# Optimization experiments

Hardware: AMD Instinct MI355X
Metric: run time of the kernel (lower is better)

Reference implementation:

```python
import jax, jax.numpy as jnp
import numpy as np

N = 50000      # nodes
E = 800000     # edges (avg degree 16)
G = 1024       # graphs in batch
C = 128        # hidden / interaction channels
FIN = 16       # num_node_features
FE = 3         # num_edge_features
L = 3          # num_interactions
CUTOFF = 10.0
LOG2 = float(np.log(2.0))
BN_EPS = 1e-5

def ssp(v):
    # ShiftedSoftplus: softplus(x) - log(2)
    return jax.nn.softplus(v) - LOG2

def setup_inputs() -> dict:
    key = jax.random.key(0)
    ks = jax.random.split(key, 24)
    s = 0.05
    inp = {}
    inp["x"] = jax.random.normal(ks[0], (N, FIN), jnp.float32)
    inp["edge_index"] = jax.random.randint(ks[1], (2, E), 0, N, dtype=jnp.int32)
    inp["edge_weight"] = jax.random.uniform(ks[2], (E,), jnp.float32) * CUTOFF
    inp["edge_attr"] = jax.random.normal(ks[3], (E, FE), jnp.float32)
    inp["batch"] = jnp.sort(jax.random.randint(ks[4], (N,), 0, G, dtype=jnp.int32))
    # node embedding (node_data='x'): Linear(FIN,C) -> Linear(C,C)
    inp["W_l1"] = jax.random.normal(ks[5], (FIN, C), jnp.float32) * s
    inp["b_l1"] = jnp.zeros((C,), jnp.float32)
    inp["W_l2"] = jax.random.normal(ks[6], (C, C), jnp.float32) * s
    inp["b_l2"] = jnp.zeros((C,), jnp.float32)
    # BatchNorm1d affine params
    inp["bn_g"] = jnp.ones((C,), jnp.float32)
    inp["bn_b"] = jnp.zeros((C,), jnp.float32)
    # L stacked interaction layers (SchNet-style CFConv)
    inp["Wi_in"] = jax.random.normal(ks[7], (L, C, C), jnp.float32) * s
    inp["bi_in"] = jnp.zeros((L, C), jnp.float32)
    inp["We1"] = jax.random.normal(ks[8], (L, FE, C), jnp.float32) * s
    inp["be1"] = jnp.zeros((L, C), jnp.float32)
    inp["We2"] = jax.random.normal(ks[9], (L, C, C), jnp.float32) * s
    inp["be2"] = jnp.zeros((L, C), jnp.float32)
    inp["Wi_out"] = jax.random.normal(ks[10], (L, C, C), jnp.float32) * s
    inp["bi_out"] = jnp.zeros((L, C), jnp.float32)
    # GeneralReadOutLayer (128,'sum',32,1): pool -> Linear(128,32)+SSP -> Linear(32,1)+SSP
    inp["W_r1"] = jax.random.normal(ks[11], (C, 32), jnp.float32) * s
    inp["b_r1"] = jnp.zeros((32,), jnp.float32)
    inp["W_r2"] = jax.random.normal(ks[12], (32, 1), jnp.float32) * s
    inp["b_r2"] = jnp.zeros((1,), jnp.float32)
    return inp

def _forward(x, edge_weight, edge_attr,
             W_l1, b_l1, W_l2, b_l2, bn_g, bn_b,
             Wi_in, bi_in, We1, be1, We2, be2, Wi_out, bi_out,
             W_r1, b_r1, W_r2, b_r2, edge_index, batch):
    src, dst = edge_index[0], edge_index[1]
    # node embedding: Linear -> Linear
    h = (x @ W_l1 + b_l1) @ W_l2 + b_l2                   # [N, C]
    # BatchNorm1d (training-mode batch stats over nodes)
    mu = jnp.mean(h, axis=0)
    var = jnp.var(h, axis=0)
    h = (h - mu) * jax.lax.rsqrt(var + BN_EPS) * bn_g + bn_b
    # cosine cutoff envelope on edge distances
    env = 0.5 * (jnp.cos(edge_weight * (jnp.pi / CUTOFF)) + 1.0)  # [E]
    # GeoResNet: residual stack of interactions
    for i in range(L):
        filt = ssp(edge_attr @ We1[i] + be1[i]) @ We2[i] + be2[i]   # [E, C]
        hin = h @ Wi_in[i] + bi_in[i]                               # [N, C]
        msg = hin[src] * filt * env[:, None]                        # [E, C] gather
        agg = jax.ops.segment_sum(msg, dst, num_segments=N)         # [N, C] scatter
        h = h + ssp(agg @ Wi_out[i] + bi_out[i])
    # GeneralReadOutLayer: segment 'sum' pool then MLP with SSP
    hg = jax.ops.segment_sum(h, batch, num_segments=G)              # [G, C]
    out = ssp(hg @ W_r1 + b_r1)
    out = ssp(out @ W_r2 + b_r2)                                    # [G, 1]
    return out.reshape(-1)                                          # [G]

def reference(x, edge_index, edge_weight, edge_attr, batch,
              W_l1, b_l1, W_l2, b_l2, bn_g, bn_b,
              Wi_in, bi_in, We1, be1, We2, be2, Wi_out, bi_out,
              W_r1, b_r1, W_r2, b_r2):
    return _forward(x, edge_weight, edge_attr,
                    W_l1, b_l1, W_l2, b_l2, bn_g, bn_b,
                    Wi_in, bi_in, We1, be1, We2, be2, Wi_out, bi_out,
                    W_r1, b_r1, W_r2, b_r2, edge_index, batch)
```

## Files before the change

kernel.cpp:

```cpp
#include <hip/hip_runtime.h>
#include <hip/hip_bf16.h>
#include <math.h>

#define N_NODES 50000
#define N_EDGES 800000
#define N_GRAPH 1024
#define CDIM 128
#define FINDIM 16
#define NL 3
#define WTP 132

using short8  = __attribute__((ext_vector_type(8))) short;
using floatx4 = __attribute__((ext_vector_type(4))) float;

__device__ __forceinline__ float sspf(float x) {
    return __logf(1.0f + __expf(x)) - 0.6931471805599453f;
}

__device__ __forceinline__ unsigned short f2bf(float f) {
    unsigned int u = __float_as_uint(f);
    u = u + 0x7FFFu + ((u >> 16) & 1u);
    return (unsigned short)(u >> 16);
}

__device__ __forceinline__ float bf2f(unsigned short h) {
    return __uint_as_float((unsigned int)h << 16);
}

__device__ __forceinline__ unsigned int packbf(float a, float b) {
    __hip_bfloat162 h = __float22bfloat162_rn(make_float2(a, b));
    return *(unsigned int*)&h;
}

__device__ __forceinline__ short8 ldfrag(const unsigned short* WT, int c, int k0) {
    const uint2* p = (const uint2*)(WT + c * WTP + k0);
    short8 r;
    *(uint2*)&r       = p[0];
    *((uint2*)&r + 1) = p[1];
    return r;
}

__global__ void k_fuse(const float* __restrict__ Wl1, const float* __restrict__ bl1,
                       const float* __restrict__ Wl2, const float* __restrict__ bl2,
                       float* __restrict__ Wf, float* __restrict__ bfv) {
    for (int o = threadIdx.x; o < FINDIM * CDIM + CDIM; o += 256) {
        if (o < FINDIM * CDIM) {
            int f = o >> 7, c = o & 127;
            float s = 0.f;
            for (int k = 0; k < CDIM; ++k) s += Wl1[f * CDIM + k] * Wl2[k * CDIM + c];
            Wf[o] = s;
        } else {
            int c = o - FINDIM * CDIM;
            float s = bl2[c];
            for (int k = 0; k < CDIM; ++k) s += bl1[k] * Wl2[k * CDIM + c];
            bfv[c] = s;
        }
    }
}

__global__ void k_embed_bn(const float* __restrict__ x, const float* __restrict__ Wf,
                           const float* __restrict__ bfv, float* __restrict__ h,
                           float* __restrict__ bnsum) {
    __shared__ float wfs[FINDIM * CDIM];
    __shared__ float bfs[CDIM];
    __shared__ float sd[512];
    for (int o = threadIdx.x; o < FINDIM * CDIM; o += 256) wfs[o] = Wf[o];
    if (threadIdx.x < CDIM) bfs[threadIdx.x] = bfv[threadIdx.x];
    __syncthreads();
    int c = threadIdx.x & 127;
    int half = threadIdx.x >> 7;
    float s1 = 0.f, s2 = 0.f;
    for (int base = blockIdx.x * 2; base < N_NODES; base += gridDim.x * 2) {
        int n = base + half;
        if (n < N_NODES) {
            float s = bfs[c];
            const float* xp = x + (size_t)n * FINDIM;
#pragma unroll
            for (int f = 0; f < FINDIM; ++f) s += xp[f] * wfs[f * CDIM + c];
            h[(size_t)n * CDIM + c] = s;
            s1 += s; s2 += s * s;
        }
    }
    sd[threadIdx.x] = s1; sd[256 + threadIdx.x] = s2;
    __syncthreads();
    if (threadIdx.x < 128) {
        atomicAdd(&bnsum[threadIdx.x], sd[threadIdx.x] + sd[threadIdx.x + 128]);
        atomicAdd(&bnsum[128 + threadIdx.x], sd[256 + threadIdx.x] + sd[256 + threadIdx.x + 128]);
    }
}

__global__ void k_bnapply(float* __restrict__ h, unsigned short* __restrict__ hb,
                          const float* __restrict__ bnsum,
                          const float* __restrict__ g, const float* __restrict__ b) {
    const float invN = 1.0f / (float)N_NODES;
    for (size_t i = (size_t)blockIdx.x * 256 + threadIdx.x; i < (size_t)N_NODES * CDIM;
         i += (size_t)gridDim.x * 256) {
        int c = (int)(i & 127);
        float mu  = bnsum[c] * invN;
        float var = bnsum[128 + c] * invN - mu * mu;
        float sc  = g[c] * rsqrtf(var + 1e-5f);
        float v = (h[i] - mu) * sc + b[c];
        h[i] = v;
        hb[i] = f2bf(v);
    }
}

__global__ void k_hist(const int* __restrict__ edst, int* __restrict__ deg) {
    int e = blockIdx.x * 256 + threadIdx.x;
    if (e < N_EDGES) atomicAdd(&deg[edst[e]], 1);
}

#define SCAN_T 1024
#define CHUNK 49
__global__ void k_scan(const int* __restrict__ deg, int* __restrict__ row_ptr) {
    __shared__ int part[SCAN_T];
    int t = threadIdx.x;
    int begin = t * CHUNK;
    int end   = begin + CHUNK; if (end > N_NODES) end = N_NODES;
    int s = 0;
    for (int i = begin; i < end && i < N_NODES; ++i) s += deg[i];
    part[t] = s;
    __syncthreads();
    for (int off = 1; off < SCAN_T; off <<= 1) {
        int v = (t >= off) ? part[t - off] : 0;
        __syncthreads();
        part[t] += v;
        __syncthreads();
    }
    int run = (t == 0) ? 0 : part[t - 1];
    for (int i = begin; i < end && i < N_NODES; ++i) { row_ptr[i] = run; run += deg[i]; }
    if (t == SCAN_T - 1) row_ptr[N_NODES] = run;
}

__global__ void k_scatter(const int* __restrict__ edst, const int* __restrict__ row_ptr,
                          int* __restrict__ cnt, int* __restrict__ perm) {
    int e = blockIdx.x * 256 + threadIdx.x;
    if (e < N_EDGES) {
        int d = edst[e];
        int pos = row_ptr[d] + atomicAdd(&cnt[d], 1);
        perm[pos] = e;
    }
}

__global__ void k_pack(const int* __restrict__ perm, const int* __restrict__ esrc,
                       const int* __restrict__ edst, const float* __restrict__ ew,
                       const float* __restrict__ ea,
                       int2* __restrict__ rmeta, float4* __restrict__ rea) {
    int i = blockIdx.x * 256 + threadIdx.x;
    if (i < N_EDGES) {
        int e = perm[i];
        float w = ew[e];
        float env = 0.5f * (__cosf(w * 0.31415926535897932f) + 1.0f);
        rmeta[i] = make_int2(esrc[e], edst[e]);
        rea[i] = make_float4(ea[(size_t)e * 3], ea[(size_t)e * 3 + 1], ea[(size_t)e * 3 + 2], env);
    }
}

__global__ __launch_bounds__(256, 2) void k_ngemm_in(const unsigned short* __restrict__ hb,
                                                     const float* __restrict__ B,
                                                     const float* __restrict__ bias,
                                                     unsigned short* __restrict__ hinb) {
    __shared__ unsigned short WT[128 * WTP];
    __shared__ float bs[CDIM];
    for (int o = threadIdx.x; o < CDIM * CDIM; o += 256) {
        int k = o >> 7, c = o & 127;
        WT[c * WTP + k] = f2bf(B[o]);
    }
    if (threadIdx.x < CDIM) bs[threadIdx.x] = bias[threadIdx.x];
    __syncthreads();

    int lane = threadIdx.x & 63, wave = threadIdx.x >> 6;
    int m = lane & 15, q = lane >> 4;
    int rb = blockIdx.x * 64 + wave * 16;
    int row = rb + m;
    if (row > N_NODES - 1) row = N_NODES - 1;

    floatx4 acc[8];
#pragma unroll
    for (int nt = 0; nt < 8; ++nt) acc[nt] = (floatx4){0.f, 0.f, 0.f, 0.f};

#pragma unroll
    for (int kb = 0; kb < 4; ++kb) {
        int k0 = kb * 32 + q * 8;
        short8 af = *(const short8*)(hb + (size_t)row * CDIM + k0);
#pragma unroll
        for (int nt = 0; nt < 8; ++nt) {
            short8 bf = ldfrag(WT, nt * 16 + m, k0);
            acc[nt] = __builtin_amdgcn_mfma_f32_16x16x32_bf16(af, bf, acc[nt], 0, 0, 0);
        }
    }
#pragma unroll
    for (int nt = 0; nt < 8; ++nt) {
        int c = nt * 16 + m;
#pragma unroll
        for (int r = 0; r < 4; ++r) {
            int orow = rb + q * 4 + r;
            if (orow < N_NODES)
                hinb[(size_t)orow * CDIM + c] = f2bf(acc[nt][r] + bs[c]);
        }
    }
}

template <int ZERO, int POOL>
__global__ __launch_bounds__(256, 2) void k_ngemm_out(float* __restrict__ agg,
                                                      const float* __restrict__ B,
                                                      const float* __restrict__ bias,
                                                      float* __restrict__ h,
                                                      unsigned short* __restrict__ hb,
                                                      const int* __restrict__ batch,
                                                      float* __restrict__ hg) {
    __shared__ unsigned short WT[128 * WTP];
    __shared__ float bs[CDIM];
    for (int o = threadIdx.x; o < CDIM * CDIM; o += 256) {
        int k = o >> 7, c = o & 127;
        WT[c * WTP + k] = f2bf(B[o]);
    }
    if (threadIdx.x < CDIM) bs[threadIdx.x] = bias[threadIdx.x];
    __syncthreads();

    int lane = threadIdx.x & 63, wave = threadIdx.x >> 6;
    int m = lane & 15, q = lane >> 4;
    int rb = blockIdx.x * 64 + wave * 16;
    int row = rb + m;
    if (row > N_NODES - 1) row = N_NODES - 1;

    floatx4 acc[8];
#pragma unroll
    for (int nt = 0; nt < 8; ++nt) acc[nt] = (floatx4){0.f, 0.f, 0.f, 0.f};

#pragma unroll
    for (int kb = 0; kb < 4; ++kb) {
        int k0 = kb * 32 + q * 8;
        const float* ap = agg + (size_t)row * CDIM + k0;
        float4 lo = *(const float4*)ap;
        float4 hi = *(const float4*)(ap + 4);
        short8 af;
        ((unsigned int*)&af)[0] = packbf(lo.x, lo.y);
        ((unsigned int*)&af)[1] = packbf(lo.z, lo.w);
        ((unsigned int*)&af)[2] = packbf(hi.x, hi.y);
        ((unsigned int*)&af)[3] = packbf(hi.z, hi.w);
#pragma unroll
        for (int nt = 0; nt < 8; ++nt) {
            short8 bf = ldfrag(WT, nt * 16 + m, k0);
            acc[nt] = __builtin_amdgcn_mfma_f32_16x16x32_bf16(af, bf, acc[nt], 0, 0, 0);
        }
    }

    int batchr[4];
    if (POOL) {
#pragma unroll
        for (int r = 0; r < 4; ++r) {
            int orow = rb + q * 4 + r;
            batchr[r] = (orow < N_NODES) ? batch[orow] : 0;
        }
    }
#pragma unroll
    for (int nt = 0; nt < 8; ++nt) {
        int c = nt * 16 + m;
#pragma unroll
        for (int r = 0; r < 4; ++r) {
            int orow = rb + q * 4 + r;
            if (orow < N_NODES) {
                size_t idx = (size_t)orow * CDIM + c;
                float hn = h[idx] + sspf(acc[nt][r] + bs[c]);
                if (POOL) {
                    atomicAdd(&hg[(size_t)batchr[r] * CDIM + c], hn);
                } else {
                    h[idx] = hn;
                    hb[idx] = f2bf(hn);
                }
                if (ZERO) agg[idx] = 0.f;
            }
        }
    }
}

__global__ __launch_bounds__(256, 4) void k_edge(
    const float* __restrict__ We1, const float* __restrict__ be1,
    const float* __restrict__ We2, const float* __restrict__ be2,
    const int2* __restrict__ rmeta, const float4* __restrict__ rea,
    const unsigned short* __restrict__ hin, float* __restrict__ agg) {
    __shared__ unsigned short WT[128 * WTP];
    __shared__ float4 we1i[CDIM];
    __shared__ float  be2s[CDIM];
    __shared__ int2   sds[64];
    __shared__ float4 eas4[64];

    for (int o = threadIdx.x; o < CDIM * CDIM; o += 256) {
        int k = o >> 7, c = o & 127;
        WT[c * WTP + k] = f2bf(We2[o]);
    }
    if (threadIdx.x < CDIM) {
        int k = threadIdx.x;
        we1i[k] = make_float4(We1[k], We1[CDIM + k], We1[2 * CDIM + k], be1[k]);
        be2s[k] = be2[k];
    }
    __syncthreads();

    int lane = threadIdx.x & 63, wave = threadIdx.x >> 6;
    int m = lane & 15, q = lane >> 4;

    float biasr[8];
#pragma unroll
    for (int nt = 0; nt < 8; ++nt) biasr[nt] = be2s[nt * 16 + m];

    const int ntiles = N_EDGES / 64;
    int tpb = (ntiles + gridDim.x - 1) / gridDim.x;
    int t0 = blockIdx.x * tpb;
    int t1 = t0 + tpb; if (t1 > ntiles) t1 = ntiles;

    for (int tile = t0; tile < t1; ++tile) {
        int s0 = tile * 64;
        __syncthreads();
        if (threadIdx.x < 64)       sds[threadIdx.x]       = rmeta[s0 + threadIdx.x];
        else if (threadIdx.x < 128) eas4[threadIdx.x - 64] = rea[s0 + threadIdx.x - 64];
        __syncthreads();

        int el0 = wave * 16 + q * 4;
        int2 sd[4]; float ev[4];
#pragma unroll
        for (int r = 0; r < 4; ++r) { sd[r] = sds[el0 + r]; ev[r] = eas4[el0 + r].w; }

        unsigned short hpre[4][8];
#pragma unroll
        for (int r = 0; r < 4; ++r) {
            const unsigned short* hp = hin + (size_t)sd[r].x * CDIM + m;
#pragma unroll
            for (int nt = 0; nt < 8; ++nt) hpre[r][nt] = hp[nt * 16];
        }

        float4 eav = eas4[wave * 16 + m];
        float ea0 = eav.x, ea1 = eav.y, ea2 = eav.z;
        short8 af[4];
#pragma unroll
        for (int kb = 0; kb < 4; ++kb) {
#pragma unroll
            for (int jj = 0; jj < 4; ++jj) {
                int k = kb * 32 + q * 8 + jj * 2;
                float4 w0 = we1i[k];
                float4 w1 = we1i[k + 1];
                float p0 = fmaf(w0.x, ea0, fmaf(w0.y, ea1, fmaf(w0.z, ea2, w0.w)));
                float p1 = fmaf(w1.x, ea0, fmaf(w1.y, ea1, fmaf(w1.z, ea2, w1.w)));
                ((unsigned int*)&af[kb])[jj] = packbf(sspf(p0), sspf(p1));
            }
        }

        floatx4 acc[8];
#pragma unroll
        for (int nt = 0; nt < 8; ++nt)
            acc[nt] = (floatx4){biasr[nt], biasr[nt], biasr[nt], biasr[nt]};
#pragma unroll
        for (int kb = 0; kb < 4; ++kb)
#pragma unroll
            for (int nt = 0; nt < 8; ++nt) {
                short8 bf = ldfrag(WT, nt * 16 + m, kb * 32 + q * 8);
                acc[nt] = __builtin_amdgcn_mfma_f32_16x16x32_bf16(af[kb], bf, acc[nt], 0, 0, 0);
            }

        bool uni = (sd[0].y == sd[3].y);
        float vv[8];
#pragma unroll
        for (int nt = 0; nt < 8; ++nt) {
            float s = 0.f;
#pragma unroll
            for (int r = 0; r < 4; ++r)
                s += acc[nt][r] * ev[r] * bf2f(hpre[r][nt]);
            vv[nt] = s;
        }

        int owner = uni ? 1 : 0;
        int myd   = uni ? sd[0].y : -1 - lane;
#pragma unroll
        for (int s = 16; s <= 32; s <<= 1) {
            int od = __shfl_xor(myd, s, 64);
            int oo = __shfl_xor(owner, s, 64);
            bool match = owner && oo && (od == myd);
            bool lower = ((lane & s) == 0);
#pragma unroll
            for (int nt = 0; nt < 8; ++nt) {
                float ovv = __shfl_xor(vv[nt], s, 64);
                if (match && lower) vv[nt] += ovv;
            }
            if (match && !lower) { owner = 0; myd = -1 - lane; }
        }

        if (uni) {
            if (owner) {
                float* ap = agg + (size_t)myd * CDIM + m;
#pragma unroll
                for (int nt = 0; nt < 8; ++nt) atomicAdd(&ap[nt * 16], vv[nt]);
            }
        } else {
#pragma unroll
            for (int nt = 0; nt < 8; ++nt) {
                int c = nt * 16 + m;
                int cur = sd[0].y;
                float accv = acc[nt][0] * ev[0] * bf2f(hpre[0][nt]);
#pragma unroll
                for (int r = 1; r < 4; ++r) {
                    float msg = acc[nt][r] * ev[r] * bf2f(hpre[r][nt]);
                    if (sd[r].y != cur) {
                        atomicAdd(&agg[(size_t)cur * CDIM + c], accv);
                        cur = sd[r].y; accv = msg;
                    } else {
                        accv += msg;
                    }
                }
                atomicAdd(&agg[(size_t)cur * CDIM + c], accv);
            }
        }
    }
}

__global__ void k_readout(const float* __restrict__ hg, const float* __restrict__ Wr1,
                          const float* __restrict__ br1, const float* __restrict__ Wr2,
                          const float* __restrict__ br2, float* __restrict__ out) {
    __shared__ float hgs[CDIM];
    int g = blockIdx.x;
    for (int o = threadIdx.x; o < CDIM; o += 64) hgs[o] = hg[(size_t)g * CDIM + o];
    __syncthreads();
    int c = threadIdx.x;
    float val = 0.f;
    if (c < 32) {
        float s = br1[c];
        for (int k = 0; k < CDIM; ++k) s += hgs[k] * Wr1[k * 32 + c];
        val = sspf(s) * Wr2[c];
    }
#pragma unroll
    for (int off = 16; off >= 1; off >>= 1) val += __shfl_down(val, off, 32);
    if (c == 0) out[g] = sspf(val + br2[0]);
}

extern "C" void kernel_launch(void* const* d_in, const int* in_sizes, int n_in,
                              void* d_out, int out_size, void* d_ws, size_t ws_size,
                              hipStream_t stream) {
    const float* x     = (const float*)d_in[0];
    const int*   eidx  = (const int*)  d_in[1];
    const float* ew    = (const float*)d_in[2];
    const float* ea    = (const float*)d_in[3];
    const int*   batch = (const int*)  d_in[4];
    const float* Wl1   = (const float*)d_in[5];
    const float* bl1   = (const float*)d_in[6];
    const float* Wl2   = (const float*)d_in[7];
    const float* bl2   = (const float*)d_in[8];
    const float* bng   = (const float*)d_in[9];
    const float* bnb   = (const float*)d_in[10];
    const float* Wi_in = (const float*)d_in[11];
    const float* bi_in = (const float*)d_in[12];
    const float* We1   = (const float*)d_in[13];
    const float* be1   = (const float*)d_in[14];
    const float* We2   = (const float*)d_in[15];
    const float* be2   = (const float*)d_in[16];
    const float* Wi_o  = (const float*)d_in[17];
    const float* bi_o  = (const float*)d_in[18];
    const float* Wr1   = (const float*)d_in[19];
    const float* br1   = (const float*)d_in[20];
    const float* Wr2   = (const float*)d_in[21];
    const float* br2   = (const float*)d_in[22];
    float* out = (float*)d_out;

    float* ws  = (float*)d_ws;
    float*  h    = ws;
    float*  agg  = h + (size_t)N_NODES * CDIM;
    float4* rea  = (float4*)(agg + (size_t)N_NODES * CDIM);
    float*  hg   = (float*)(rea + N_EDGES);
    float*  Wf   = hg + (size_t)N_GRAPH * CDIM;
    float*  bfv  = Wf + FINDIM * CDIM;
    float*  bnsum = bfv + CDIM;
    unsigned short* hb   = (unsigned short*)(bnsum + 256);
    unsigned short* hinb = hb + (size_t)N_NODES * CDIM;
    int2*  rmeta  = (int2*)(hinb + (size_t)N_NODES * CDIM);
    int*   perm   = (int*)(rmeta + N_EDGES);
    int*   deg    = perm + N_EDGES;
    int*   row_ptr= deg + N_NODES;
    int*   cnt    = row_ptr + N_NODES + 1;

    const int* esrc = eidx;
    const int* edst = eidx + N_EDGES;

    hipMemsetAsync(deg, 0, (size_t)N_NODES * sizeof(int), stream);
    hipMemsetAsync(cnt, 0, (size_t)N_NODES * sizeof(int), stream);
    k_hist<<<(N_EDGES + 255) / 256, 256, 0, stream>>>(edst, deg);
    k_scan<<<1, SCAN_T, 0, stream>>>(deg, row_ptr);
    k_scatter<<<(N_EDGES + 255) / 256, 256, 0, stream>>>(edst, row_ptr, cnt, perm);
    k_pack<<<(N_EDGES + 255) / 256, 256, 0, stream>>>(perm, esrc, edst, ew, ea, rmeta, rea);

    hipMemsetAsync(bnsum, 0, 256 * sizeof(float), stream);
    k_fuse<<<1, 256, 0, stream>>>(Wl1, bl1, Wl2, bl2, Wf, bfv);
    k_embed_bn<<<512, 256, 0, stream>>>(x, Wf, bfv, h, bnsum);
    k_bnapply<<<1024, 256, 0, stream>>>(h, hb, bnsum, bng, bnb);

    hipMemsetAsync(agg, 0, (size_t)N_NODES * CDIM * sizeof(float), stream);
    hipMemsetAsync(hg, 0, (size_t)N_GRAPH * CDIM * sizeof(float), stream);
    const int ngrid = (N_NODES + 63) / 64;
    for (int l = 0; l < NL; ++l) {
        k_ngemm_in<<<ngrid, 256, 0, stream>>>(hb, Wi_in + (size_t)l * CDIM * CDIM,
                                              bi_in + l * CDIM, hinb);
        k_edge<<<1024, 256, 0, stream>>>(We1 + l * 3 * CDIM, be1 + l * CDIM,
                                         We2 + (size_t)l * CDIM * CDIM, be2 + l * CDIM,
                                         rmeta, rea, hinb, agg);
        if (l < NL - 1)
            k_ngemm_out<1, 0><<<ngrid, 256, 0, stream>>>(agg, Wi_o + (size_t)l * CDIM * CDIM,
                                                         bi_o + l * CDIM, h, hb, batch, hg);
        else
            k_ngemm_out<0, 1><<<ngrid, 256, 0, stream>>>(agg, Wi_o + (size_t)l * CDIM * CDIM,
                                                         bi_o + l * CDIM, h, hb, batch, hg);
    }

    k_readout<<<N_GRAPH, 64, 0, stream>>>(hg, Wr1, br1, Wr2, br2, out);
}
```

Before: 985.6 us.

## Fuse output GEMM with next layer's input GEMM via shared-memory node tile

For the first two layers, the output-projection kernel now also computes the next layer's input projection. The updated node tile is kept in LDS as bf16, so the bf16 copy of h is no longer written and read back, and one kernel launch per layer is saved. The single-block weight-fusion kernel is also spread over 9 blocks. The cost is roughly double the LDS per block, which may lower occupancy, plus a second weight staging and an extra barrier inside each block.

```diff
diff --git a/kernel.cpp b/kernel.cpp
--- a/kernel.cpp
+++ b/kernel.cpp
@@ -32,8 +32,8 @@
     return *(unsigned int*)&h;
 }
 
-__device__ __forceinline__ short8 ldfrag(const unsigned short* WT, int c, int k0) {
-    const uint2* p = (const uint2*)(WT + c * WTP + k0);
+__device__ __forceinline__ short8 ldfrag(const unsigned short* T, int row, int k0) {
+    const uint2* p = (const uint2*)(T + row * WTP + k0);
     short8 r;
     *(uint2*)&r       = p[0];
     *((uint2*)&r + 1) = p[1];
@@ -43,18 +43,19 @@
 __global__ void k_fuse(const float* __restrict__ Wl1, const float* __restrict__ bl1,
                        const float* __restrict__ Wl2, const float* __restrict__ bl2,
                        float* __restrict__ Wf, float* __restrict__ bfv) {
-    for (int o = threadIdx.x; o < FINDIM * CDIM + CDIM; o += 256) {
-        if (o < FINDIM * CDIM) {
-            int f = o >> 7, c = o & 127;
-            float s = 0.f;
-            for (int k = 0; k < CDIM; ++k) s += Wl1[f * CDIM + k] * Wl2[k * CDIM + c];
-            Wf[o] = s;
-        } else {
-            int c = o - FINDIM * CDIM;
-            float s = bl2[c];
-            for (int k = 0; k < CDIM; ++k) s += bl1[k] * Wl2[k * CDIM + c];
-            bfv[c] = s;
-        }
+    int o = blockIdx.x * 256 + threadIdx.x;
+    if (o < FINDIM * CDIM) {
+        int f = o >> 7, c = o & 127;
+        float s = 0.f;
+#pragma unroll 4
+        for (int k = 0; k < CDIM; ++k) s += Wl1[f * CDIM + k] * Wl2[k * CDIM + c];
+        Wf[o] = s;
+    } else if (o < FINDIM * CDIM + CDIM) {
+        int c = o - FINDIM * CDIM;
+        float s = bl2[c];
+#pragma unroll 4
+        for (int k = 0; k < CDIM; ++k) s += bl1[k] * Wl2[k * CDIM + c];
+        bfv[c] = s;
     }
 }
 
@@ -201,21 +202,23 @@
     }
 }
 
-template <int ZERO, int POOL>
-__global__ __launch_bounds__(256, 2) void k_ngemm_out(float* __restrict__ agg,
-                                                      const float* __restrict__ B,
-                                                      const float* __restrict__ bias,
-                                                      float* __restrict__ h,
-                                                      unsigned short* __restrict__ hb,
-                                                      const int* __restrict__ batch,
-                                                      float* __restrict__ hg) {
+__global__ __launch_bounds__(256, 2) void k_fused_oi(float* __restrict__ agg,
+                                                     const float* __restrict__ Bo,
+                                                     const float* __restrict__ bo,
+                                                     float* __restrict__ h,
+                                                     const float* __restrict__ Bi,
+                                                     const float* __restrict__ bi,
+                                                     unsigned short* __restrict__ hinb) {
     __shared__ unsigned short WT[128 * WTP];
-    __shared__ float bs[CDIM];
+    __shared__ unsigned short hnS[64 * WTP];
+    __shared__ float bso[CDIM];
+    __shared__ float bsi[CDIM];
+
     for (int o = threadIdx.x; o < CDIM * CDIM; o += 256) {
         int k = o >> 7, c = o & 127;
-        WT[c * WTP + k] = f2bf(B[o]);
-    }
-    if (threadIdx.x < CDIM) bs[threadIdx.x] = bias[threadIdx.x];
+        WT[c * WTP + k] = f2bf(Bo[o]);
+    }
+    if (threadIdx.x < CDIM) { bso[threadIdx.x] = bo[threadIdx.x]; bsi[threadIdx.x] = bi[threadIdx.x]; }
     __syncthreads();
 
     int lane = threadIdx.x & 63, wave = threadIdx.x >> 6;
@@ -246,13 +249,104 @@
         }
     }
 
-    int batchr[4];
-    if (POOL) {
+#pragma unroll
+    for (int nt = 0; nt < 8; ++nt) {
+        int c = nt * 16 + m;
+#pragma unroll
+        for (int r = 0; r < 4; ++r) {
+            int lrow = wave * 16 + q * 4 + r;
+            int orow = rb + q * 4 + r;
+            if (orow < N_NODES) {
+                size_t idx = (size_t)orow * CDIM + c;
+                float hn = h[idx] + sspf(acc[nt][r] + bso[c]);
+                h[idx] = hn;
+                agg[idx] = 0.f;
+                hnS[lrow * WTP + c] = f2bf(hn);
+            } else {
+                hnS[lrow * WTP + c] = 0;
+            }
+        }
+    }
+    __syncthreads();
+
+    for (int o = threadIdx.x; o < CDIM * CDIM; o += 256) {
+        int k = o >> 7, c = o & 127;
+        WT[c * WTP + k] = f2bf(Bi[o]);
+    }
+    __syncthreads();
+
+#pragma unroll
+    for (int nt = 0; nt < 8; ++nt) acc[nt] = (floatx4){0.f, 0.f, 0.f, 0.f};
+#pragma unroll
+    for (int kb = 0; kb < 4; ++kb) {
+        int k0 = kb * 32 + q * 8;
+        short8 af = ldfrag(hnS, wave * 16 + m, k0);
+#pragma unroll
+        for (int nt = 0; nt < 8; ++nt) {
+            short8 bf = ldfrag(WT, nt * 16 + m, k0);
+            acc[nt] = __builtin_amdgcn_mfma_f32_16x16x32_bf16(af, bf, acc[nt], 0, 0, 0);
+        }
+    }
+#pragma unroll
+    for (int nt = 0; nt < 8; ++nt) {
+        int c = nt * 16 + m;
 #pragma unroll
         for (int r = 0; r < 4; ++r) {
             int orow = rb + q * 4 + r;
-            batchr[r] = (orow < N_NODES) ? batch[orow] : 0;
-        }
+            if (orow < N_NODES)
+                hinb[(size_t)orow * CDIM + c] = f2bf(acc[nt][r] + bsi[c]);
+        }
+    }
+}
+
+__global__ __launch_bounds__(256, 2) void k_ngemm_out_pool(const float* __restrict__ agg,
+                                                           const float* __restrict__ B,
+                                                           const float* __restrict__ bias,
+                                                           const float* __restrict__ h,
+                                                           const int* __restrict__ batch,
+                                                           float* __restrict__ hg) {
+    __shared__ unsigned short WT[128 * WTP];
+    __shared__ float bs[CDIM];
+    for (int o = threadIdx.x; o < CDIM * CDIM; o += 256) {
+        int k = o >> 7, c = o & 127;
+        WT[c * WTP + k] = f2bf(B[o]);
+    }
+    if (threadIdx.x < CDIM) bs[threadIdx.x] = bias[threadIdx.x];
+    __syncthreads();
+
+    int lane = threadIdx.x & 63, wave = threadIdx.x >> 6;
+    int m = lane & 15, q = lane >> 4;
+    int rb = blockIdx.x * 64 + wave * 16;
+    int row = rb + m;
+    if (row > N_NODES - 1) row = N_NODES - 1;
+
+    floatx4 acc[8];
+#pragma unroll
+    for (int nt = 0; nt < 8; ++nt) acc[nt] = (floatx4){0.f, 0.f, 0.f, 0.f};
+
+#pragma unroll
+    for (int kb = 0; kb < 4; ++kb) {
+        int k0 = kb * 32 + q * 8;
+        const float* ap = agg + (size_t)row * CDIM + k0;
+        float4 lo = *(const float4*)ap;
+        float4 hi = *(const float4*)(ap + 4);
+        short8 af;
+        ((unsigned int*)&af)[0] = packbf(lo.x, lo.y);
+        ((unsigned int*)&af)[1] = packbf(lo.z, lo.w);
+        ((unsigned int*)&af)[2] = packbf(hi.x, hi.y);
+        ((unsigned int*)&af)[3] = packbf(hi.z, hi.w);
+#pragma unroll
+        for (int nt = 0; nt < 8; ++nt) {
+            short8 bf = ldfrag(WT, nt * 16 + m, k0);
+            acc[nt] = __builtin_amdgcn_mfma_f32_16x16x32_bf16(af, bf, acc[nt], 0, 0, 0);
+        }
+    }
+
+    int batchr[4];
+#pragma unroll
+    for (int r = 0; r < 4; ++r) {
+        int orow = rb + q * 4 + r;
+        batchr[r] = (orow < N_NODES) ? batch[orow] : 0;
     }
 #pragma unroll
     for (int nt = 0; nt < 8; ++nt) {
@@ -263,13 +357,7 @@
             if (orow < N_NODES) {
                 size_t idx = (size_t)orow * CDIM + c;
                 float hn = h[idx] + sspf(acc[nt][r] + bs[c]);
-                if (POOL) {
-                    atomicAdd(&hg[(size_t)batchr[r] * CDIM + c], hn);
-                } else {
-                    h[idx] = hn;
-                    hb[idx] = f2bf(hn);
-                }
-                if (ZERO) agg[idx] = 0.f;
+                atomicAdd(&hg[(size_t)batchr[r] * CDIM + c], hn);
             }
         }
     }
@@ -486,25 +574,27 @@
     k_pack<<<(N_EDGES + 255) / 256, 256, 0, stream>>>(perm, esrc, edst, ew, ea, rmeta, rea);
 
     hipMemsetAsync(bnsum, 0, 256 * sizeof(float), stream);
-    k_fuse<<<1, 256, 0, stream>>>(Wl1, bl1, Wl2, bl2, Wf, bfv);
+    k_fuse<<<9, 256, 0, stream>>>(Wl1, bl1, Wl2, bl2, Wf, bfv);
     k_embed_bn<<<512, 256, 0, stream>>>(x, Wf, bfv, h, bnsum);
     k_bnapply<<<1024, 256, 0, stream>>>(h, hb, bnsum, bng, bnb);
 
     hipMemsetAsync(agg, 0, (size_t)N_NODES * CDIM * sizeof(float), stream);
     hipMemsetAsync(hg, 0, (size_t)N_GRAPH * CDIM * sizeof(float), stream);
     const int ngrid = (N_NODES + 63) / 64;
+
+    k_ngemm_in<<<ngrid, 256, 0, stream>>>(hb, Wi_in, bi_in, hinb);
     for (int l = 0; l < NL; ++l) {
-        k_ngemm_in<<<ngrid, 256, 0, stream>>>(hb, Wi_in + (size_t)l * CDIM * CDIM,
-                                              bi_in + l * CDIM, hinb);
         k_edge<<<1024, 256, 0, stream>>>(We1 + l * 3 * CDIM, be1 + l * CDIM,
                                          We2 + (size_t)l * CDIM * CDIM, be2 + l * CDIM,
                                          rmeta, rea, hinb, agg);
         if (l < NL - 1)
-            k_ngemm_out<1, 0><<<ngrid, 256, 0, stream>>>(agg, Wi_o + (size_t)l * CDIM * CDIM,
-                                                         bi_o + l * CDIM, h, hb, batch, hg);
+            k_fused_oi<<<ngrid, 256, 0, stream>>>(agg, Wi_o + (size_t)l * CDIM * CDIM,
+                                                  bi_o + l * CDIM, h,
+                                                  Wi_in + (size_t)(l + 1) * CDIM * CDIM,
+                                                  bi_in + (l + 1) * CDIM, hinb);
         else
-            k_ngemm_out<0, 1><<<ngrid, 256, 0, stream>>>(agg, Wi_o + (size_t)l * CDIM * CDIM,
-                                                         bi_o + l * CDIM, h, hb, batch, hg);
+            k_ngemm_out_pool<<<ngrid, 256, 0, stream>>>(agg, Wi_o + (size_t)l * CDIM * CDIM,
+                                                        bi_o + l * CDIM, h, batch, hg);
     }
 
     k_readout<<<N_GRAPH, 64, 0, stream>>>(hg, Wr1, br1, Wr2, br2, out);
```

After: 985.7 us. Within noise of the previous version (+0.0%).
